# Optimization experiments

Hardware: AMD Instinct MI355X
Metric: run time of the kernel (lower is better)

Reference implementation:

```python
import jax, jax.numpy as jnp
import numpy as np

MAXTIME = 1406073600
MINTIME = 832550400
SPAN = 10000
TIME_EMB = 100
N_GATE = 8
NUM_INTEREST = 4
DIM = 64
SEQ = 256
BATCH = 1024
ALPHA = 0.1
PI = 3.14159  # matches the literal in the source


def _build_time_table():
    # TimeEncoder: interleaved sin/cos positional table over time buckets.
    n = MAXTIME // SPAN + 3
    pos = np.arange(n, dtype=np.float64)[:, None]
    div = np.exp(np.arange(TIME_EMB // 2, dtype=np.float64) * -(np.log(10000.0) / TIME_EMB))[None, :]
    te = np.zeros((n, TIME_EMB), dtype=np.float32)
    te[:, 0::2] = np.sin(pos * div)
    te[:, 1::2] = np.cos(pos * div)
    return jnp.asarray(te)

_TIME_TABLE = _build_time_table()


def _time_encode(t):
    idx = (t / SPAN).astype(jnp.int32)
    return _TIME_TABLE[idx - jnp.min(idx)]


def setup_inputs() -> dict:
    key = jax.random.key(0)
    ks = jax.random.split(key, 11)
    B, S, D, NI, G = BATCH, SEQ, DIM, NUM_INTEREST, N_GATE
    item_his_emb = jax.random.normal(ks[0], (B, S, D), jnp.float32)
    item_eb = jax.random.normal(ks[1], (B, D), jnp.float32)
    # query times near maxtime, history times strictly earlier -> positive deltas
    t_batch = MAXTIME - 1e6 * jax.random.uniform(ks[2], (B,), jnp.float32)
    t_his = MINTIME + (MAXTIME - MINTIME - 1e6) * jax.random.uniform(ks[3], (B, S), jnp.float32)
    mask = (jax.random.uniform(ks[4], (B, S)) > 0.3).astype(jnp.float32)
    W1 = jax.random.normal(ks[5], (3 * TIME_EMB, 100), jnp.float32) / np.sqrt(3 * TIME_EMB)
    b1 = jnp.zeros((100,), jnp.float32)
    W2 = jax.random.normal(ks[6], (100, 1), jnp.float32) * 0.1
    b2 = jnp.zeros((1,), jnp.float32)
    phase = 100000.0 * jax.random.uniform(ks[7], (1, 1, G), jnp.float32)
    tao = 86400.0 * jnp.array([[[1, 2, 7, 14, 30, 60, 365, 730]]], jnp.float32)
    ratio = 0.3 * jax.random.uniform(ks[8], (1, 1, G), jnp.float32)
    gate_emb = jax.random.normal(ks[9], (1, D, G), jnp.float32)
    w_bilinear = jax.random.normal(ks[10], (S, NI * D, D), jnp.float32)
    return {"item_his_emb": item_his_emb, "item_eb": item_eb, "t_batch": t_batch,
            "t_his": t_his, "mask": mask, "W1": W1, "b1": b1, "W2": W2, "b2": b2,
            "phase": phase, "tao": tao, "ratio": ratio, "gate_emb": gate_emb,
            "w_bilinear": w_bilinear, "ta": 2}


def reference(item_his_emb, item_eb, t_batch, t_his, mask, W1, b1, W2, b2,
              phase, tao, ratio, gate_emb, w_bilinear, ta):
    B, S, D = item_his_emb.shape
    NI = NUM_INTEREST
    # --- time factor ---
    t_tiled = jnp.broadcast_to(t_batch[:, None], (B, S))
    time_feature = jnp.concatenate([_time_encode(t_tiled), _time_encode(t_his),
                                    _time_encode(t_tiled - t_his)], axis=2)  # [B,S,300]
    hidden1 = jax.nn.relu(time_feature @ W1 + b1)
    t_factor = jnp.transpose(jax.nn.sigmoid(hidden1 @ W2 + b2), (0, 2, 1))  # [B,1,S]
    # --- circadian gate factor ---
    phi = jnp.mod(t_his[:, :, None] - phase, tao) / tao  # [B,S,G]
    gate = jnp.where(phi < ratio, jnp.maximum(jnp.sin(PI * phi / ratio), 0.0), ALPHA * phi)
    gate_ratio = jax.nn.softmax(jnp.einsum('bsd,dg->bsg', item_his_emb, gate_emb[0]), axis=2) * gate
    g_factor = jnp.sum(gate_ratio, axis=2)[:, None, :]  # [B,1,S]
    reg1 = jnp.linalg.norm(t_factor)
    reg2 = jnp.linalg.norm(ratio) + jnp.linalg.norm(phase) / 100000.0
    # ta == 2 branch
    loss_reg = 0.1 * reg1 + 1.0 * reg2 + 1.0 / reg1 + 0.1 / reg2
    factor = jnp.broadcast_to(t_factor + g_factor, (B, NI, S))
    # --- bilinear_type == 2 projection ---
    item_emb_hat = jnp.einsum('skd,bsd->bsk', w_bilinear, item_his_emb)  # [B,S,NI*D]
    item_emb_hat = item_emb_hat.reshape(B, S, NI, D).transpose(0, 2, 1, 3)  # [B,NI,S,D]
    hat_iter = jax.lax.stop_gradient(item_emb_hat)
    # --- dynamic routing, 3 iterations ---
    cw = jnp.zeros((B, NI, S), item_his_emb.dtype)
    amask = mask[:, None, :]
    cap = None
    for i in range(3):
        sw = jax.nn.softmax(cw, axis=1)           # softmax over interests
        sw = jnp.where(amask == 0, 0.0, sw)
        src = hat_iter if i < 2 else item_emb_hat
        cap = jnp.einsum('bks,bksd->bkd', sw, src)  # [B,NI,D]
        n2 = jnp.sum(cap * cap, axis=-1, keepdims=True)
        cap = (n2 / (1.0 + n2) / jnp.sqrt(n2 + 1e-9)) * cap  # squash
        if i < 2:
            delta = jnp.einsum('bksd,bkd->bks', hat_iter, cap) * factor
            cw = cw + delta
    interest_capsule = cap  # [B,NI,D]
    # --- hard readout ---
    atten = jax.nn.softmax(jnp.einsum('bkd,bd->bk', interest_capsule, item_eb), axis=1)
    readout = interest_capsule[jnp.arange(B), jnp.argmax(atten, axis=1)]  # [B,D]
    return interest_capsule, readout, loss_reg
```

## Files before the change

### kernel.cpp

```cpp
#include <hip/hip_runtime.h>
#include <math.h>
#include <limits.h>

#define BB 1024
#define SS 256
#define DD 64
#define NI 4
#define NG 8
#define TE_N 100
#define PMAX 57420
#define ROWP 100
#define TPB 16

#define OFF_FTH   ((size_t)0)
#define OFF_FDF   ((size_t)PMAX*ROWP)
#define OFF_GTB   ((size_t)2*PMAX*ROWP)
#define OFF_FAC   (OFF_GTB + (size_t)BB*ROWP)
#define OFF_SCAL  (OFF_FAC + (size_t)BB*SS)
#define OFF_GFT   (OFF_SCAL + 32)
#define OFF_HAT   (OFF_GFT + (size_t)BB*SS)

__global__ void k_init(float* ws){
    if (threadIdx.x == 0){
        int* mi = (int*)(ws + OFF_SCAL);
        mi[0] = INT_MAX; mi[1] = INT_MAX; mi[2] = INT_MAX;
        ws[OFF_SCAL + 4] = 0.0f;
    }
}

__global__ void k_min(const float* __restrict__ tb, const float* __restrict__ th, float* ws){
    int gid = blockIdx.x * blockDim.x + threadIdx.x;
    int stride = gridDim.x * blockDim.x;
    int m0 = INT_MAX, m1 = INT_MAX, m2 = INT_MAX;
    for (int i = gid; i < BB*SS; i += stride){
        float t  = th[i];
        float t2 = tb[i >> 8];
        int i1 = (int)(t / 10000.0f);
        int i2 = (int)((t2 - t) / 10000.0f);
        m1 = min(m1, i1);
        m2 = min(m2, i2);
    }
    if (gid < BB) m0 = (int)(tb[gid] / 10000.0f);
    #pragma unroll
    for (int off = 1; off < 64; off <<= 1){
        m0 = min(m0, __shfl_xor(m0, off));
        m1 = min(m1, __shfl_xor(m1, off));
        m2 = min(m2, __shfl_xor(m2, off));
    }
    if ((threadIdx.x & 63) == 0){
        int* mi = (int*)(ws + OFF_SCAL);
        atomicMin(mi + 0, m0);
        atomicMin(mi + 1, m1);
        atomicMin(mi + 2, m2);
    }
}

__global__ void k_tables(const float* __restrict__ W1, float* ws){
    int pbase = blockIdx.x * TPB;
    int t = threadIdx.x;
    __shared__ float te[TPB][TE_N];
    for (int idx = t; idx < TPB*50; idx += 128){
        int pp = idx / 50, h = idx - pp*50;
        double div = exp((double)h * -0.09210340371976184);
        double a = (double)(pbase + pp) * div;
        te[pp][2*h]   = (float)sin(a);
        te[pp][2*h+1] = (float)cos(a);
    }
    __syncthreads();
    if (t < TE_N){
        float a1[TPB], a2[TPB];
        #pragma unroll
        for (int pp = 0; pp < TPB; pp++){ a1[pp] = 0.f; a2[pp] = 0.f; }
        for (int i = 0; i < TE_N; i++){
            float w1v = W1[(100+i)*100 + t];
            float w2v = W1[(200+i)*100 + t];
            #pragma unroll
            for (int pp = 0; pp < TPB; pp++){
                float v = te[pp][i];
                a1[pp] += v * w1v;
                a2[pp] += v * w2v;
            }
        }
        for (int pp = 0; pp < TPB; pp++){
            int p = pbase + pp;
            if (p < PMAX){
                ws[OFF_FTH + (size_t)p*ROWP + t] = a1[pp];
                ws[OFF_FDF + (size_t)p*ROWP + t] = a2[pp];
            }
        }
    }
}

__global__ void k_gtb(const float* __restrict__ tb, const float* __restrict__ W1,
                      const float* __restrict__ b1, float* ws){
    int b = blockIdx.x;
    int t = threadIdx.x;
    const int* mi = (const int*)(ws + OFF_SCAL);
    int p = (int)(tb[b] / 10000.0f) - mi[0];
    __shared__ float te[TE_N];
    if (t < TE_N/2){
        double div = exp((double)t * -0.09210340371976184);
        double a = (double)p * div;
        te[2*t]   = (float)sin(a);
        te[2*t+1] = (float)cos(a);
    }
    __syncthreads();
    if (t < TE_N){
        float a1 = b1[t];
        for (int i = 0; i < TE_N; i++) a1 += te[i] * W1[i*100 + t];
        ws[OFF_GTB + (size_t)b*ROWP + t] = a1;
    }
}

__global__ void __launch_bounds__(256) k_factor(const float* __restrict__ tbatch,
                         const float* __restrict__ th_, const float* __restrict__ W2,
                         const float* __restrict__ b2, float* ws){
    int b  = blockIdx.x >> 1;
    int sh = blockIdx.x & 1;
    int t  = threadIdx.x;
    int lane = t & 63, wv = t >> 6;
    __shared__ float sgtb[TE_N];
    if (t < TE_N) sgtb[t] = ws[OFF_GTB + (size_t)b*ROWP + t];
    __syncthreads();

    bool tail = (lane < 36);
    float w2a = W2[lane];
    float w2b = tail ? W2[64 + lane] : 0.f;
    float ga  = sgtb[lane];
    float gb  = tail ? sgtb[64 + lane] : 0.f;
    float bias = b2[0];

    int sbase = sh*128 + wv*32;
    const int* mi = (const int*)(ws + OFF_SCAL);
    int pth = 0, pdf = 0;
    if (lane < 32){
        float thv = th_[(size_t)b*SS + sbase + lane];
        float tbv = tbatch[b];
        pth = (int)(thv / 10000.0f) - mi[1];
        pdf = (int)((tbv - thv) / 10000.0f) - mi[2];
        pth = min(max(pth, 0), PMAX-1);
        pdf = min(max(pdf, 0), PMAX-1);
    }

    float tfkeep = 0.f;
    float r1acc  = 0.f;
    #pragma unroll 4
    for (int i = 0; i < 32; i++){
        int p1 = __shfl(pth, i);
        int p2 = __shfl(pdf, i);
        const float* r1 = ws + OFF_FTH + (size_t)p1*ROWP;
        const float* r2 = ws + OFF_FDF + (size_t)p2*ROWP;
        float a  = r1[lane];
        float c  = r2[lane];
        float a2 = tail ? r1[64 + lane] : 0.f;
        float c2 = tail ? r2[64 + lane] : 0.f;
        float h = fmaxf(ga + a + c, 0.f) * w2a;
        if (tail) h += fmaxf(gb + a2 + c2, 0.f) * w2b;
        #pragma unroll
        for (int off = 1; off < 64; off <<= 1) h += __shfl_xor(h, off);
        float tf = 1.f / (1.f + expf(-(h + bias)));
        if (lane == i){ tfkeep = tf; r1acc += tf*tf; }
    }
    if (lane < 32) ws[OFF_FAC + (size_t)b*SS + sbase + lane] = tfkeep;
    #pragma unroll
    for (int off = 1; off < 64; off <<= 1) r1acc += __shfl_xor(r1acc, off);
    if (lane == 0) atomicAdd(ws + OFF_SCAL + 4, r1acc);
}

__global__ void __launch_bounds__(256, 2)
k_hat(const float* __restrict__ X, const float* __restrict__ Wb,
      const float* __restrict__ th_, const float* __restrict__ phase,
      const float* __restrict__ tao, const float* __restrict__ ratio,
      const float* __restrict__ ge, float* __restrict__ hat,
      float* __restrict__ gfT, int b0, int nb){
    int btile = blockIdx.x;
    int s     = blockIdx.y;
    int t     = threadIdx.x;

    __shared__ float xs[128][68];
    __shared__ float wl[128][68];
    __shared__ float sge[NG][65];
    __shared__ float sth[128];
    __shared__ float glog[128][9];

    int rows = nb - btile*128; if (rows > 128) rows = 128;

    const float* xbase = X + ((size_t)(b0 + btile*128)*SS + s)*DD;
    for (int q = t; q < 2048; q += 256){
        int r = q >> 4, jf = q & 15;
        if (r < rows)
            ((float4*)&xs[r][0])[jf] = *(const float4*)(xbase + (size_t)r*SS*DD + jf*4);
    }
    for (int i = t; i < DD*NG; i += 256) sge[i & 7][i >> 3] = ge[i];
    if (t < 128 && t < rows) sth[t] = th_[(size_t)(b0 + btile*128 + t)*SS + s];
    __syncthreads();

    for (int task = t; task < 1024; task += 256){
        int r = task >> 3, g = task & 7;
        if (r < rows){
            float acc = 0.f;
            #pragma unroll
            for (int d = 0; d < DD; d++) acc += xs[r][d] * sge[g][d];
            glog[r][g] = acc;
        }
    }
    __syncthreads();

    int tx = t & 15;
    int ty = t >> 4;

    for (int kdh = 0; kdh < 2; kdh++){
        if (kdh == 1) __syncthreads();
        const float4* wsrc = (const float4*)(Wb + (size_t)s*16384 + (size_t)kdh*8192);
        for (int q = t; q < 2048; q += 256){
            int kd = q >> 4, jf = q & 15;
            ((float4*)&wl[kd][0])[jf] = wsrc[q];
        }
        if (kdh == 0 && t < 128 && t < rows){
            int r = t;
            float lg[NG];
            #pragma unroll
            for (int g = 0; g < NG; g++) lg[g] = glog[r][g];
            float mx = lg[0];
            #pragma unroll
            for (int g = 1; g < NG; g++) mx = fmaxf(mx, lg[g]);
            float e[NG]; float es = 0.f;
            #pragma unroll
            for (int g = 0; g < NG; g++){ e[g] = expf(lg[g]-mx); es += e[g]; }
            float thv = sth[r];
            float gf = 0.f;
            #pragma unroll
            for (int g = 0; g < NG; g++){
                float phv = fmodf(thv - phase[g], tao[g]) / tao[g];
                float gv = (phv < ratio[g]) ? fmaxf(sinf(3.14159f*phv/ratio[g]), 0.f) : 0.1f*phv;
                gf += (e[g]/es) * gv;
            }
            gfT[(size_t)s*BB + (b0 + btile*128 + r)] = gf;
        }
        __syncthreads();

        float acc[8][8];
        #pragma unroll
        for (int i = 0; i < 8; i++)
            #pragma unroll
            for (int m = 0; m < 8; m++) acc[i][m] = 0.f;

        for (int jq = 0; jq < 16; jq++){
            float4 xv[8], wv[8];
            #pragma unroll
            for (int i = 0; i < 8; i++) xv[i] = ((const float4*)&xs[ty + 16*i][0])[jq];
            #pragma unroll
            for (int m = 0; m < 8; m++) wv[m] = ((const float4*)&wl[tx + 16*m][0])[jq];
            #pragma unroll
            for (int i = 0; i < 8; i++){
                #pragma unroll
                for (int m = 0; m < 8; m++){
                    acc[i][m] += xv[i].x*wv[m].x + xv[i].y*wv[m].y
                               + xv[i].z*wv[m].z + xv[i].w*wv[m].w;
                }
            }
        }

        #pragma unroll
        for (int i = 0; i < 8; i++){
            int r = ty + 16*i;
            if (r < rows){
                size_t base = ((size_t)(btile*128 + r)*SS + s)*256 + (size_t)kdh*128;
                #pragma unroll
                for (int m = 0; m < 8; m++)
                    hat[base + tx + 16*m] = acc[i][m];
            }
        }
    }
}

__global__ void __launch_bounds__(1024) k_route(const float* __restrict__ eb,
                                                const float* __restrict__ mask_,
                                                const float* __restrict__ ws,
                                                const float* __restrict__ hat,
                                                float* __restrict__ out, int b0){
    int bl = blockIdx.x;
    int b = b0 + bl;
    int t = threadIdx.x;
    int lane = t & 63, wv = t >> 6, k = t & 3;
    __shared__ float part[16][4][64];
    __shared__ float capl[4][68];
    __shared__ float logits[4];
    __shared__ int kms;

    float hat_r[64];
    const float4* hsrc = (const float4*)(hat + (size_t)bl*65536 + (size_t)t*64);
    #pragma unroll
    for (int jc = 0; jc < 16; jc++){
        float4 v = hsrc[jc];
        hat_r[4*jc] = v.x; hat_r[4*jc+1] = v.y; hat_r[4*jc+2] = v.z; hat_r[4*jc+3] = v.w;
    }
    int s = t >> 2;
    float fac = ws[OFF_FAC + (size_t)b*SS + s] + ws[OFF_GFT + (size_t)s*BB + b];
    float mk = mask_[b*SS + s];
    float cw = 0.f;
    float capv = 0.f;

    for (int it = 0; it < 3; ++it){
        float m = fmaxf(cw, __shfl_xor(cw, 1)); m = fmaxf(m, __shfl_xor(m, 2));
        float e = expf(cw - m);
        float ssum = e + __shfl_xor(e, 1); ssum += __shfl_xor(ssum, 2);
        float sw = (mk == 0.f) ? 0.f : (e / ssum);

        #pragma unroll
        for (int c = 0; c < 4; c++){
            float tmp[16];
            #pragma unroll
            for (int i = 0; i < 16; i++) tmp[i] = sw * hat_r[c*16 + i];
            #pragma unroll
            for (int msk = 4; msk < 64; msk <<= 1){
                #pragma unroll
                for (int i = 0; i < 16; i++) tmp[i] += __shfl_xor(tmp[i], msk);
            }
            if (lane < 4){
                #pragma unroll
                for (int i = 0; i < 16; i++) part[wv][lane][c*16 + i] = tmp[i];
            }
        }
        __syncthreads();
        if (t < 256){
            int k2 = t >> 6, d = t & 63;
            float cp = 0.f;
            #pragma unroll
            for (int w2 = 0; w2 < 16; w2++) cp += part[w2][k2][d];
            float q = cp * cp;
            #pragma unroll
            for (int msk = 1; msk < 64; msk <<= 1) q += __shfl_xor(q, msk);
            float sc = q / ((1.f + q) * sqrtf(q + 1e-9f));
            capv = sc * cp;
            capl[k2][d] = capv;
        }
        __syncthreads();
        if (it < 2){
            const float4* cp4 = (const float4*)&capl[k][0];
            float dot = 0.f;
            #pragma unroll
            for (int jc = 0; jc < 16; jc++){
                float4 v = cp4[jc];
                dot += hat_r[4*jc]*v.x + hat_r[4*jc+1]*v.y + hat_r[4*jc+2]*v.z + hat_r[4*jc+3]*v.w;
            }
            cw += dot * fac;
        }
        __syncthreads();
    }

    if (t < 256){
        int k2 = t >> 6, d = t & 63;
        out[(size_t)b*256 + t] = capv;
        float qq = capv * eb[b*DD + d];
        #pragma unroll
        for (int msk = 1; msk < 64; msk <<= 1) qq += __shfl_xor(qq, msk);
        if (lane == 0) logits[k2] = qq;
    }
    __syncthreads();
    if (t == 0){
        float best = logits[0]; int km = 0;
        for (int kk = 1; kk < 4; kk++) if (logits[kk] > best){ best = logits[kk]; km = kk; }
        kms = km;
    }
    __syncthreads();
    if (t < 64) out[(size_t)BB*256 + (size_t)b*64 + t] = capl[kms][t];
}

__global__ void k_final(const float* __restrict__ phase, const float* __restrict__ ratio,
                        float* ws, float* __restrict__ out){
    if (threadIdx.x == 0){
        float r2a = 0.f, r2b = 0.f;
        for (int g = 0; g < NG; g++){ r2a += ratio[g]*ratio[g]; r2b += phase[g]*phase[g]; }
        float reg2 = sqrtf(r2a) + sqrtf(r2b) / 100000.0f;
        float reg1 = sqrtf(ws[OFF_SCAL + 4]);
        out[(size_t)BB*256 + (size_t)BB*64] = 0.1f*reg1 + reg2 + 1.0f/reg1 + 0.1f/reg2;
    }
}

extern "C" void kernel_launch(void* const* d_in, const int* in_sizes, int n_in,
                              void* d_out, int out_size, void* d_ws, size_t ws_size,
                              hipStream_t stream){
    const float* Xh = (const float*)d_in[0];
    const float* eb = (const float*)d_in[1];
    const float* tb = (const float*)d_in[2];
    const float* th = (const float*)d_in[3];
    const float* mk = (const float*)d_in[4];
    const float* W1 = (const float*)d_in[5];
    const float* b1 = (const float*)d_in[6];
    const float* W2 = (const float*)d_in[7];
    const float* b2 = (const float*)d_in[8];
    const float* ph = (const float*)d_in[9];
    const float* ta = (const float*)d_in[10];
    const float* ra = (const float*)d_in[11];
    const float* ge = (const float*)d_in[12];
    const float* wb = (const float*)d_in[13];
    float* out = (float*)d_out;
    float* ws  = (float*)d_ws;

    hipLaunchKernelGGL(k_init,   dim3(1),    dim3(64),  0, stream, ws);
    hipLaunchKernelGGL(k_min,    dim3(256),  dim3(256), 0, stream, tb, th, ws);
    hipLaunchKernelGGL(k_tables, dim3((PMAX+TPB-1)/TPB), dim3(128), 0, stream, W1, ws);
    hipLaunchKernelGGL(k_gtb,    dim3(BB),   dim3(128), 0, stream, tb, W1, b1, ws);
    hipLaunchKernelGGL(k_factor, dim3(2*BB), dim3(256), 0, stream, tb, th, W2, b2, ws);

    long wfloats  = (long)(ws_size / sizeof(float));
    long hatavail = wfloats - (long)OFF_HAT;
    int CH = (int)(hatavail / 65536);
    if (CH > BB) CH = BB;
    if (CH >= 128) CH &= ~127;
    if (CH < 1)  CH = 1;
    float* hatbuf = ws + OFF_HAT;
    for (int c0 = 0; c0 < BB; c0 += CH){
        int nb = BB - c0; if (nb > CH) nb = CH;
        int nbt = (nb + 127) / 128;
        hipLaunchKernelGGL(k_hat,   dim3(nbt, 256), dim3(256),  0, stream,
                           Xh, wb, th, ph, ta, ra, ge, hatbuf, ws + OFF_GFT, c0, nb);
        hipLaunchKernelGGL(k_route, dim3(nb),       dim3(1024), 0, stream, eb, mk, ws, hatbuf, out, c0);
    }
    hipLaunchKernelGGL(k_final, dim3(1), dim3(64), 0, stream, ph, ra, ws, out);
}
```

Baseline: 611.9 us.

## Split gate softmax into own kernel and retile k_hat for 512 threads

The per-position gate factor (softmax over gate logits times the periodic gate value) moves out of the hat GEMM kernel into a new k_gate kernel, which adds it straight into the FAC buffer. That removes the separate GFT buffer and the extra read in k_route. k_hat becomes a pure GEMM with 512 threads, an 8x4 accumulator tile per thread, and the second half of the weight matrix prefetched into registers while the first half is computed. The intent is to cut per-thread register pressure and GEMM serialization to raise occupancy. The cost is one extra launch and a second pass that re-reads X for the gate logits.

```diff
diff --git a/kernel.cpp b/kernel.cpp
--- a/kernel.cpp
+++ b/kernel.cpp
@@ -17,8 +17,7 @@
 #define OFF_GTB   ((size_t)2*PMAX*ROWP)
 #define OFF_FAC   (OFF_GTB + (size_t)BB*ROWP)
 #define OFF_SCAL  (OFF_FAC + (size_t)BB*SS)
-#define OFF_GFT   (OFF_SCAL + 32)
-#define OFF_HAT   (OFF_GFT + (size_t)BB*SS)
+#define OFF_HAT   (OFF_SCAL + 32)
 
 __global__ void k_init(float* ws){
     if (threadIdx.x == 0){
@@ -167,94 +166,104 @@
     if (lane == 0) atomicAdd(ws + OFF_SCAL + 4, r1acc);
 }
 
-__global__ void __launch_bounds__(256, 2)
-k_hat(const float* __restrict__ X, const float* __restrict__ Wb,
+__global__ void __launch_bounds__(256) k_gate(const float* __restrict__ X,
       const float* __restrict__ th_, const float* __restrict__ phase,
       const float* __restrict__ tao, const float* __restrict__ ratio,
-      const float* __restrict__ ge, float* __restrict__ hat,
-      float* __restrict__ gfT, int b0, int nb){
+      const float* __restrict__ ge, float* ws){
+    __shared__ float sge[NG][DD];
+    int t = threadIdx.x;
+    for (int i = t; i < DD*NG; i += 256) sge[i & 7][i >> 3] = ge[i];
+    __syncthreads();
+    int gid = blockIdx.x * 256 + t;
+
+    float lg[NG];
+    #pragma unroll
+    for (int g = 0; g < NG; g++) lg[g] = 0.f;
+    const float4* xr = (const float4*)(X + (size_t)gid*DD);
+    #pragma unroll 4
+    for (int dc = 0; dc < 16; dc++){
+        float4 xv = xr[dc];
+        #pragma unroll
+        for (int g = 0; g < NG; g++){
+            lg[g] += xv.x*sge[g][dc*4+0] + xv.y*sge[g][dc*4+1]
+                   + xv.z*sge[g][dc*4+2] + xv.w*sge[g][dc*4+3];
+        }
+    }
+    float mx = lg[0];
+    #pragma unroll
+    for (int g = 1; g < NG; g++) mx = fmaxf(mx, lg[g]);
+    float thv = th_[gid];
+    float es = 0.f, gf = 0.f;
+    #pragma unroll
+    for (int g = 0; g < NG; g++){
+        float e = expf(lg[g] - mx);
+        es += e;
+        float phv = fmodf(thv - phase[g], tao[g]) / tao[g];
+        float gv = (phv < ratio[g]) ? fmaxf(sinf(3.14159f*phv/ratio[g]), 0.f) : 0.1f*phv;
+        gf += e * gv;
+    }
+    ws[OFF_FAC + gid] += gf / es;
+}
+
+__global__ void __launch_bounds__(512, 2)
+k_hat(const float* __restrict__ X, const float* __restrict__ Wb,
+      float* __restrict__ hat, int b0, int nb){
     int btile = blockIdx.x;
     int s     = blockIdx.y;
     int t     = threadIdx.x;
 
     __shared__ float xs[128][68];
     __shared__ float wl[128][68];
-    __shared__ float sge[NG][65];
-    __shared__ float sth[128];
-    __shared__ float glog[128][9];
 
     int rows = nb - btile*128; if (rows > 128) rows = 128;
 
     const float* xbase = X + ((size_t)(b0 + btile*128)*SS + s)*DD;
-    for (int q = t; q < 2048; q += 256){
+    for (int q = t; q < 2048; q += 512){
         int r = q >> 4, jf = q & 15;
         if (r < rows)
             ((float4*)&xs[r][0])[jf] = *(const float4*)(xbase + (size_t)r*SS*DD + jf*4);
     }
-    for (int i = t; i < DD*NG; i += 256) sge[i & 7][i >> 3] = ge[i];
-    if (t < 128 && t < rows) sth[t] = th_[(size_t)(b0 + btile*128 + t)*SS + s];
-    __syncthreads();
-
-    for (int task = t; task < 1024; task += 256){
-        int r = task >> 3, g = task & 7;
-        if (r < rows){
-            float acc = 0.f;
-            #pragma unroll
-            for (int d = 0; d < DD; d++) acc += xs[r][d] * sge[g][d];
-            glog[r][g] = acc;
-        }
-    }
-    __syncthreads();
-
-    int tx = t & 15;
-    int ty = t >> 4;
+    const float4* wsrc = (const float4*)(Wb + (size_t)s*16384);
+    for (int q = t; q < 2048; q += 512){
+        int kd = q >> 4, jf = q & 15;
+        ((float4*)&wl[kd][0])[jf] = wsrc[q];
+    }
+    __syncthreads();
+
+    int tx = t & 31;
+    int ty = t >> 5;
+    float4 pre[4];
 
     for (int kdh = 0; kdh < 2; kdh++){
-        if (kdh == 1) __syncthreads();
-        const float4* wsrc = (const float4*)(Wb + (size_t)s*16384 + (size_t)kdh*8192);
-        for (int q = t; q < 2048; q += 256){
-            int kd = q >> 4, jf = q & 15;
-            ((float4*)&wl[kd][0])[jf] = wsrc[q];
-        }
-        if (kdh == 0 && t < 128 && t < rows){
-            int r = t;
-            float lg[NG];
-            #pragma unroll
-            for (int g = 0; g < NG; g++) lg[g] = glog[r][g];
-            float mx = lg[0];
-            #pragma unroll
-            for (int g = 1; g < NG; g++) mx = fmaxf(mx, lg[g]);
-            float e[NG]; float es = 0.f;
-            #pragma unroll
-            for (int g = 0; g < NG; g++){ e[g] = expf(lg[g]-mx); es += e[g]; }
-            float thv = sth[r];
-            float gf = 0.f;
-            #pragma unroll
-            for (int g = 0; g < NG; g++){
-                float phv = fmodf(thv - phase[g], tao[g]) / tao[g];
-                float gv = (phv < ratio[g]) ? fmaxf(sinf(3.14159f*phv/ratio[g]), 0.f) : 0.1f*phv;
-                gf += (e[g]/es) * gv;
-            }
-            gfT[(size_t)s*BB + (b0 + btile*128 + r)] = gf;
-        }
-        __syncthreads();
-
-        float acc[8][8];
+        if (kdh == 0){
+            #pragma unroll
+            for (int pq = 0; pq < 4; pq++) pre[pq] = wsrc[2048 + t + 512*pq];
+        } else {
+            __syncthreads();
+            #pragma unroll
+            for (int pq = 0; pq < 4; pq++){
+                int q = t + 512*pq;
+                ((float4*)&wl[q >> 4][0])[q & 15] = pre[pq];
+            }
+            __syncthreads();
+        }
+
+        float acc[8][4];
         #pragma unroll
         for (int i = 0; i < 8; i++)
             #pragma unroll
-            for (int m = 0; m < 8; m++) acc[i][m] = 0.f;
+            for (int m = 0; m < 4; m++) acc[i][m] = 0.f;
 
         for (int jq = 0; jq < 16; jq++){
-            float4 xv[8], wv[8];
+            float4 xv[8], wv[4];
             #pragma unroll
             for (int i = 0; i < 8; i++) xv[i] = ((const float4*)&xs[ty + 16*i][0])[jq];
             #pragma unroll
-            for (int m = 0; m < 8; m++) wv[m] = ((const float4*)&wl[tx + 16*m][0])[jq];
+            for (int m = 0; m < 4; m++) wv[m] = ((const float4*)&wl[tx + 32*m][0])[jq];
             #pragma unroll
             for (int i = 0; i < 8; i++){
                 #pragma unroll
-                for (int m = 0; m < 8; m++){
+                for (int m = 0; m < 4; m++){
                     acc[i][m] += xv[i].x*wv[m].x + xv[i].y*wv[m].y
                                + xv[i].z*wv[m].z + xv[i].w*wv[m].w;
                 }
@@ -267,8 +276,8 @@
             if (r < rows){
                 size_t base = ((size_t)(btile*128 + r)*SS + s)*256 + (size_t)kdh*128;
                 #pragma unroll
-                for (int m = 0; m < 8; m++)
-                    hat[base + tx + 16*m] = acc[i][m];
+                for (int m = 0; m < 4; m++)
+                    hat[base + tx + 32*m] = acc[i][m];
             }
         }
     }
@@ -296,7 +305,7 @@
         hat_r[4*jc] = v.x; hat_r[4*jc+1] = v.y; hat_r[4*jc+2] = v.z; hat_r[4*jc+3] = v.w;
     }
     int s = t >> 2;
-    float fac = ws[OFF_FAC + (size_t)b*SS + s] + ws[OFF_GFT + (size_t)s*BB + b];
+    float fac = ws[OFF_FAC + (size_t)b*SS + s];
     float mk = mask_[b*SS + s];
     float cw = 0.f;
     float capv = 0.f;
@@ -403,6 +412,7 @@
     hipLaunchKernelGGL(k_tables, dim3((PMAX+TPB-1)/TPB), dim3(128), 0, stream, W1, ws);
     hipLaunchKernelGGL(k_gtb,    dim3(BB),   dim3(128), 0, stream, tb, W1, b1, ws);
     hipLaunchKernelGGL(k_factor, dim3(2*BB), dim3(256), 0, stream, tb, th, W2, b2, ws);
+    hipLaunchKernelGGL(k_gate,   dim3(BB),   dim3(256), 0, stream, Xh, th, ph, ta, ra, ge, ws);
 
     long wfloats  = (long)(ws_size / sizeof(float));
     long hatavail = wfloats - (long)OFF_HAT;
@@ -414,8 +424,7 @@
     for (int c0 = 0; c0 < BB; c0 += CH){
         int nb = BB - c0; if (nb > CH) nb = CH;
         int nbt = (nb + 127) / 128;
-        hipLaunchKernelGGL(k_hat,   dim3(nbt, 256), dim3(256),  0, stream,
-                           Xh, wb, th, ph, ta, ra, ge, hatbuf, ws + OFF_GFT, c0, nb);
+        hipLaunchKernelGGL(k_hat,   dim3(nbt, 256), dim3(512),  0, stream, Xh, wb, hatbuf, c0, nb);
         hipLaunchKernelGGL(k_route, dim3(nb),       dim3(1024), 0, stream, eb, mk, ws, hatbuf, out, c0);
     }
     hipLaunchKernelGGL(k_final, dim3(1), dim3(64), 0, stream, ph, ra, ws, out);
```

Result: slower. 634.0 us (+3.6%).
